# Optimization experiments

Measured on AMD Instinct MI355X. Metric: run time of the kernel, lower is better.

## Reference

```python
import jax, jax.numpy as jnp
import numpy as np
from jax import lax

CONF_THRES = 0.5
IOU_THRES = 0.45
TOP_K = 2048  # fixed candidate cap for jit-friendly NMS


def _xywh2xyxy(x):
    # x: [N,4] center-x, center-y, w, h -> x1,y1,x2,y2
    xy, wh = x[:, :2], x[:, 2:4]
    return jnp.concatenate([xy - wh / 2, xy + wh / 2], axis=-1)


def _box_iou(b1, b2):
    # b1: [N,4], b2: [M,4] in xyxy -> [N,M]
    area1 = (b1[:, 2] - b1[:, 0]) * (b1[:, 3] - b1[:, 1])
    area2 = (b2[:, 2] - b2[:, 0]) * (b2[:, 3] - b2[:, 1])
    lt = jnp.maximum(b1[:, None, :2], b2[None, :, :2])
    rb = jnp.minimum(b1[:, None, 2:], b2[None, :, 2:])
    inter = jnp.clip(rb - lt, 0).prod(-1)
    return inter / (area1[:, None] + area2[None, :] - inter)


def _nms_per_image(x):
    # x: [N,16] = xywh(4), obj(1), landmarks(10), cls_score(1); nc=1 path
    obj = x[:, 4]
    conf = x[:, 15] * obj          # x[:,15:] *= x[:,4:5], then max over 1 class
    box = _xywh2xyxy(x[:, :4])
    valid = (obj > CONF_THRES) & (conf > CONF_THRES)
    score = jnp.where(valid, conf, -jnp.inf)

    topv, topi = lax.top_k(score, TOP_K)          # sorted descending
    valid_k = jnp.isfinite(topv)                  # [K]
    boxes_k = box[topi]                           # [K,4]; class offset c = 0 (nc=1)
    x_k = x[topi]                                 # [K,16]
    conf_k = conf[topi]

    iou = _box_iou(boxes_k, boxes_k)              # [K,K]

    def body(keep, inp):
        i, iou_row, v = inp
        suppressed = jnp.any(keep & (iou_row > IOU_THRES))
        keep_i = v & ~suppressed
        return keep.at[i].set(keep_i), keep_i

    keep, _ = lax.scan(body, jnp.zeros(TOP_K, bool),
                       (jnp.arange(TOP_K), iou, valid_k))

    # detection row: [x1,y1,x2,y2, conf, 10 landmarks, class(=0)]
    det = jnp.concatenate(
        [boxes_k, conf_k[:, None], x_k[:, 5:15],
         jnp.zeros((TOP_K, 1), x.dtype)], axis=1)
    return jnp.where(keep[:, None], det, jnp.zeros((), x.dtype))


def setup_inputs() -> dict:
    key = jax.random.key(0)
    prediction = jax.random.uniform(key, (8, 100800, 16), dtype=jnp.float32)
    return {"prediction": prediction}


def reference(prediction):
    # prediction: [B, N, 16] -> padded detections [B, TOP_K, 16]
    return jax.vmap(_nms_per_image)(prediction)
```

## Files before the change

### kernel.cpp

```cpp
#include <hip/hip_runtime.h>
#include <stdint.h>

#define NA    100800
#define NIMG  8
#define TOPK  2048
#define NBLK1 99
typedef unsigned long long u64;

__global__ __launch_bounds__(256) void k1_scan(const float* __restrict__ pred,
                                               u64* __restrict__ cand,
                                               int* __restrict__ hist,
                                               int* __restrict__ cnt) {
    __shared__ int lhist[64];
    __shared__ u64 lkeys[1024];
    __shared__ int lcnt;
    __shared__ int gbase;
    int t = threadIdx.x;
    int m = blockIdx.y;
    if (t < 64) lhist[t] = 0;
    if (t == 0) lcnt = 0;
    __syncthreads();
    const float4* p4 = reinterpret_cast<const float4*>(pred + (size_t)m * NA * 16);
    int row0blk = blockIdx.x * 1024;
    for (int pass = 0; pass < 4; ++pass) {
        int row0 = row0blk + pass * 256;
        int i1 = row0 * 4 + 2 * t + 1;
        int i2 = i1 + 512;
        float4 A = make_float4(0.f, 0.f, 0.f, 0.f);
        float4 B = make_float4(0.f, 0.f, 0.f, 0.f);
        if ((i1 >> 2) < NA) A = p4[i1];
        if ((i2 >> 2) < NA) B = p4[i2];
        float aw = __shfl_xor(A.w, 1);
        float bw = __shfl_xor(B.w, 1);
        if (!(t & 1)) {
            int rA = row0 + (t >> 1);
            int rB = rA + 128;
            {
                float obj = A.x, x15 = aw;
                if (rA < NA) {
                    float conf = __fmul_rn(x15, obj);
                    if (obj > 0.5f && conf > 0.5f) {
                        unsigned cb = __float_as_uint(conf);
                        atomicAdd(&lhist[min(63, (int)((cb - 0x3F000000u) >> 17))], 1);
                        int p = atomicAdd(&lcnt, 1);
                        lkeys[p] = ((u64)cb << 32) | (u64)(0xFFFFFFFFu - (unsigned)rA);
                    }
                }
            }
            {
                float obj = B.x, x15 = bw;
                if (rB < NA) {
                    float conf = __fmul_rn(x15, obj);
                    if (obj > 0.5f && conf > 0.5f) {
                        unsigned cb = __float_as_uint(conf);
                        atomicAdd(&lhist[min(63, (int)((cb - 0x3F000000u) >> 17))], 1);
                        int p = atomicAdd(&lcnt, 1);
                        lkeys[p] = ((u64)cb << 32) | (u64)(0xFFFFFFFFu - (unsigned)rB);
                    }
                }
            }
        }
    }
    __syncthreads();
    if (t < 64 && lhist[t]) atomicAdd(&hist[(m << 6) + t], lhist[t]);
    if (t == 0) gbase = lcnt ? atomicAdd(&cnt[m], lcnt) : 0;
    __syncthreads();
    int n = lcnt;
    u64* cm = cand + (size_t)m * NA;
    for (int i = t; i < n; i += 256) cm[gbase + i] = lkeys[i];
}

__global__ __launch_bounds__(1024) void k2_rank(const u64* __restrict__ cand,
                                                const int* __restrict__ hist,
                                                const int* __restrict__ cnt,
                                                const float* __restrict__ pred,
                                                u64* __restrict__ sel,
                                                float4* __restrict__ boxes) {
    __shared__ int fcnt[4096];
    __shared__ int fstart[4096];
    __shared__ u64 outb[4096];
    __shared__ int wsum[16];
    __shared__ int cutsh, msh;
    int m = blockIdx.x, t = threadIdx.x;
    int lane = t & 63, w = t >> 6;
    if (t == 0) msh = 0;
    #pragma unroll
    for (int r = 0; r < 4; ++r) { fcnt[t + r * 1024] = 0; outb[t + r * 1024] = 0ull; }
    __syncthreads();
    if (w == 0) {
        int h = hist[(m << 6) + lane];
        #pragma unroll
        for (int off = 1; off < 64; off <<= 1) {
            int src = lane + off;
            int v = __shfl(h, src < 64 ? src : lane);
            h += (src < 64) ? v : 0;
        }
        int total  = __shfl(h, 0);
        int needed = min(total, TOPK);
        u64 bal = __ballot(h >= needed);
        int cutoff = 63 - __clzll(bal);
        if (lane == 0) cutsh = cutoff;
    }
    __syncthreads();
    int cut = cutsh;
    int count = cnt[m];
    const u64* cm = cand + (size_t)m * NA;
    for (int i = t; i < count; i += 1024) {
        u64 key = cm[i];
        unsigned cb = (unsigned)(key >> 32);
        bool keep = min(63, (int)((cb - 0x3F000000u) >> 17)) >= cut;
        u64 bal = __ballot(keep);
        if (bal) {
            int n = __popcll(bal);
            int base = 0;
            if (lane == 0) base = atomicAdd(&msh, n);
            base = __shfl(base, 0);
            if (keep) {
                int p = base + (int)__popcll(bal & ((1ull << lane) - 1ull));
                if (p < 4096) outb[p] = key;
            }
        }
    }
    __syncthreads();
    int M = min(msh, 4096);
    u64 kk[4]; int rb[4];
    #pragma unroll
    for (int r = 0; r < 4; ++r) {
        int i = t + r * 1024;
        kk[r] = 0ull; rb[r] = -1;
        if (i < M) {
            kk[r] = outb[i];
            rb[r] = 4095 - (int)(((unsigned)(kk[r] >> 32) - 0x3F000000u) >> 11);
            atomicAdd(&fcnt[rb[r]], 1);
        }
    }
    __syncthreads();
    int c0 = fcnt[4 * t], c1 = fcnt[4 * t + 1], c2 = fcnt[4 * t + 2], c3 = fcnt[4 * t + 3];
    int s = c0 + c1 + c2 + c3;
    int incl = s;
    #pragma unroll
    for (int off = 1; off < 64; off <<= 1) {
        int v = __shfl_up(incl, off);
        if (lane >= off) incl += v;
    }
    if (lane == 63) wsum[w] = incl;
    __syncthreads();
    if (w == 0) {
        int v = (lane < 16) ? wsum[lane] : 0;
        #pragma unroll
        for (int off = 1; off < 16; off <<= 1) {
            int u = __shfl_up(v, off);
            if (lane >= off) v += u;
        }
        if (lane < 16) wsum[lane] = v;
    }
    __syncthreads();
    int base = (w > 0 ? wsum[w - 1] : 0) + (incl - s);
    fstart[4 * t]     = base;
    fstart[4 * t + 1] = base + c0;
    fstart[4 * t + 2] = base + c0 + c1;
    fstart[4 * t + 3] = base + c0 + c1 + c2;
    __syncthreads();
    #pragma unroll
    for (int r = 0; r < 4; ++r) {
        if (rb[r] >= 0) {
            int old = atomicSub(&fcnt[rb[r]], 1);
            int slot = fstart[rb[r]] + old - 1;
            outb[slot] = kk[r];
        }
    }
    __syncthreads();
    #pragma unroll
    for (int r = 0; r < 4; ++r) {
        int b = t + r * 1024;
        int st = fstart[b];
        int en = (b < 4095) ? fstart[b + 1] : M;
        for (int x = st + 1; x < en; ++x) {
            u64 key = outb[x];
            int y = x - 1;
            while (y >= st && outb[y] < key) { outb[y + 1] = outb[y]; --y; }
            outb[y + 1] = key;
        }
    }
    __syncthreads();
    #pragma unroll
    for (int r = 0; r < 2; ++r) {
        int i = t + r * 1024;
        u64 key = outb[i];
        sel[(size_t)m * TOPK + i] = key;
        float4 b = make_float4(0.f, 0.f, 0.f, 0.f);
        if (key) {
            unsigned idx = 0xFFFFFFFFu - (unsigned)(key & 0xFFFFFFFFull);
            const float4* rv = reinterpret_cast<const float4*>(pred + ((size_t)m * NA + idx) * 16);
            float4 v = rv[0];
            float hw = __fmul_rn(v.z, 0.5f), hh = __fmul_rn(v.w, 0.5f);
            b.x = __fsub_rn(v.x, hw);
            b.y = __fsub_rn(v.y, hh);
            b.z = __fadd_rn(v.x, hw);
            b.w = __fadd_rn(v.y, hh);
        }
        boxes[(size_t)m * TOPK + i] = b;
    }
}

__global__ __launch_bounds__(1024) void k4_masks(const float4* __restrict__ boxes,
                                                 u64* __restrict__ maskT) {
    __shared__ float4 bx[TOPK];
    int m   = blockIdx.y;
    int grp = blockIdx.x;
    for (int i = threadIdx.x; i < TOPK; i += 1024)
        bx[i] = boxes[(size_t)m * TOPK + i];
    __syncthreads();

    int il = threadIdx.x & 31;
    int w  = threadIdx.x >> 5;
    int i  = grp * 32 + il;
    float4 b1 = bx[i];
    float a1 = __fmul_rn(__fsub_rn(b1.z, b1.x), __fsub_rn(b1.w, b1.y));
    u64 bits = 0ull;
    #pragma unroll 4
    for (int jj = 0; jj < 64; ++jj) {
        float4 b2 = bx[w * 64 + jj];
        float a2 = __fmul_rn(__fsub_rn(b2.z, b2.x), __fsub_rn(b2.w, b2.y));
        float iw = fmaxf(__fsub_rn(fminf(b1.z, b2.z), fmaxf(b1.x, b2.x)), 0.f);
        float ih = fmaxf(__fsub_rn(fminf(b1.w, b2.w), fmaxf(b1.y, b2.y)), 0.f);
        float inter = __fmul_rn(iw, ih);
        float uni   = __fsub_rn(__fadd_rn(a1, a2), inter);
        float iou   = __fdiv_rn(inter, uni);
        if (iou > 0.45f) bits |= (1ull << jj);
    }
    maskT[((size_t)m * 32 + w) * 2048 + i] = bits;
}

__global__ __launch_bounds__(1024) void k5_nms(const u64* __restrict__ sel,
                                               const u64* __restrict__ maskT,
                                               const float* __restrict__ pred,
                                               float4* __restrict__ out) {
    __shared__ u64 remv[32];
    __shared__ u64 kbshare[2];
    __shared__ u64 kws[32];
    int m = blockIdx.x;
    int t = threadIdx.x;
    int lane = t & 63;
    int wv = t >> 6;
    const u64* mt = maskT + (size_t)m * 32 * 2048;
    if (t < 32) remv[t] = 0ull;
    u64 dval = 0ull, sval = 0ull, tval = 0ull;
    u64 cfmask = 0ull;
    u64 mybit = 1ull << lane;
    u64 lowmask = mybit - 1ull;
    if (wv == 0) {
        dval = mt[(size_t)0 * 2048 + lane];
        sval = sel[(size_t)m * TOPK + lane];
        tval = mt[(size_t)0 * 2048 + 64 + lane];
    }
    __syncthreads();

    u64 uA1 = 0ull, uA2 = 0ull, uB1 = 0ull, uB2 = 0ull;

#define K5_SCAN(B) do {                                                       \
    u64 dn = 0ull, sn = 0ull, tn = 0ull;                                      \
    if ((B) < 31) {                                                           \
        int r = ((B) + 1) * 64 + lane;                                        \
        dn = mt[(size_t)((B) + 1) * 2048 + r];                                \
        sn = sel[(size_t)m * TOPK + r];                                       \
        if ((B) < 30) tn = mt[(size_t)((B) + 1) * 2048 + r + 64];             \
    }                                                                         \
    u64 ext = remv[(B)];                                                      \
    u64 validw = __ballot(sval != 0ull);                                      \
    u64 alive = validw & ~ext & ~cfmask;                                      \
    u64 kb = 0ull;                                                            \
    while (alive) {                                                           \
        u64 c = dval & alive & lowmask;                                       \
        u64 ready = __ballot(((alive & mybit) != 0ull) && (c == 0ull));       \
        kb |= ready;                                                          \
        u64 removed = __ballot((dval & ready) != 0ull);                       \
        alive &= ~(ready | removed);                                          \
    }                                                                         \
    cfmask = ((B) < 31) ? __ballot((tval & kb) != 0ull) : 0ull;               \
    if (lane == 0) { kbshare[(B) & 1] = kb; kws[(B)] = kb; }                  \
    dval = dn; sval = sn; tval = tn;                                          \
} while (0)

#define K5_UP_ISSUE(V1, V2, S) do {           \
    int w1_ = (S) + wv, w2_ = (S) + 15 + wv;                                  \
    V1 = (w1_ < 32) ? mt[(size_t)((S) - 1) * 2048 + w1_ * 64 + lane] : 0ull;  \
    V2 = (w2_ < 32) ? mt[(size_t)((S) - 1) * 2048 + w2_ * 64 + lane] : 0ull;  \
} while (0)

#define K5_UP_CONSUME(V1, V2, B) do {                                         \
    u64 kb = kbshare[((B) - 1) & 1];                                          \
    int w1_ = (B) + wv, w2_ = (B) + 15 + wv;                                  \
    u64 c1 = __ballot((V1 & kb) != 0ull);                                     \
    u64 c2 = __ballot((V2 & kb) != 0ull);                                     \
    if (w1_ < 32 && lane == 0) remv[w1_] |= c1;                               \
    if (w2_ < 32 && lane == 0) remv[w2_] |= c2;                               \
} while (0)

    #pragma unroll 1
    for (int it = 0; it < 16; ++it) {
        int b0 = 2 * it, b1 = b0 + 1;
        if (wv == 0) {
            K5_SCAN(b0);
        } else {
            K5_UP_ISSUE(uB1, uB2, b0 + 1);
            if (b0 >= 1) K5_UP_CONSUME(uA1, uA2, b0);
        }
        __syncthreads();
        if (wv == 0) {
            K5_SCAN(b1);
        } else {
            if (b1 + 1 < 32) K5_UP_ISSUE(uA1, uA2, b1 + 1);
            K5_UP_CONSUME(uB1, uB2, b1);
        }
        __syncthreads();
    }
#undef K5_SCAN
#undef K5_UP_ISSUE
#undef K5_UP_CONSUME

    const u64* sl = sel + (size_t)m * TOPK;
    float4* om = out + (size_t)m * TOPK * 4;
    #pragma unroll
    for (int q = t; q < TOPK * 4; q += 1024) {
        int c4 = q & 3;
        int r  = q >> 2;
        float4 o = make_float4(0.f, 0.f, 0.f, 0.f);
        if ((kws[r >> 6] >> (r & 63)) & 1ull) {
            u64 key = sl[r];
            unsigned idx = 0xFFFFFFFFu - (unsigned)(key & 0xFFFFFFFFull);
            const float4* rv = reinterpret_cast<const float4*>(pred + ((size_t)m * NA + idx) * 16);
            float4 v = rv[c4];
            if (c4 == 0) {
                float hw = __fmul_rn(v.z, 0.5f), hh = __fmul_rn(v.w, 0.5f);
                o = make_float4(__fsub_rn(v.x, hw), __fsub_rn(v.y, hh),
                                __fadd_rn(v.x, hw), __fadd_rn(v.y, hh));
            } else if (c4 == 1) {
                o = make_float4(__uint_as_float((unsigned)(key >> 32)), v.y, v.z, v.w);
            } else if (c4 == 2) {
                o = v;
            } else {
                o = make_float4(v.x, v.y, v.z, 0.f);
            }
        }
        om[q] = o;
    }
}

extern "C" void kernel_launch(void* const* d_in, const int* in_sizes, int n_in,
                              void* d_out, int out_size, void* d_ws, size_t ws_size,
                              hipStream_t stream) {
    (void)in_sizes; (void)n_in; (void)out_size; (void)ws_size;
    const float* pred = (const float*)d_in[0];
    char* ws = (char*)d_ws;
    u64*      cand     = (u64*)     (ws + 0);
    u64*      sel      = (u64*)     (ws + 6451200);
    float4*   boxes    = (float4*)  (ws + 6582272);
    u64*      maskT    = (u64*)     (ws + 6844416);
    int*      hist     = (int*)     (ws + 11038720);
    int*      cnt      = (int*)     (ws + 11040768);
    float4*   out      = (float4*)d_out;

    hipMemsetAsync(hist, 0, 2048 + 32, stream);
    hipLaunchKernelGGL(k1_scan,  dim3(NBLK1, NIMG), dim3(256),  0, stream, pred, cand, hist, cnt);
    hipLaunchKernelGGL(k2_rank,  dim3(NIMG),        dim3(1024), 0, stream, cand, hist, cnt, pred, sel, boxes);
    hipLaunchKernelGGL(k4_masks, dim3(64, NIMG),    dim3(1024), 0, stream, boxes, maskT);
    hipLaunchKernelGGL(k5_nms,   dim3(NIMG),        dim3(1024), 0, stream, sel, maskT, pred, out);
}
```

Measured before the change: 94.61 us.

## Replace global atomics with per-block histograms and shrink NMS block to 512

k1 now writes each block's 64-bin histogram and candidate count to per-block slots, and stores its keys at a fixed per-block offset instead of reserving space with global atomics. This removes the memset launch and atomic contention. k2 reduces the per-block histograms itself and walks the 99 segments, paying one extra pass with a per-segment loop that leaves most threads idle. Separately, k5 drops to 512 threads, and each updater wave now handles up to 5 mask words at stride 7 instead of 2, cutting the cost of each block-wide barrier.

```diff
diff --git a/kernel.cpp b/kernel.cpp
--- a/kernel.cpp
+++ b/kernel.cpp
@@ -9,19 +9,19 @@
 
 __global__ __launch_bounds__(256) void k1_scan(const float* __restrict__ pred,
                                                u64* __restrict__ cand,
-                                               int* __restrict__ hist,
-                                               int* __restrict__ cnt) {
+                                               int* __restrict__ histb,
+                                               int* __restrict__ bcnt) {
     __shared__ int lhist[64];
     __shared__ u64 lkeys[1024];
     __shared__ int lcnt;
-    __shared__ int gbase;
     int t = threadIdx.x;
     int m = blockIdx.y;
+    int b = blockIdx.x;
     if (t < 64) lhist[t] = 0;
     if (t == 0) lcnt = 0;
     __syncthreads();
     const float4* p4 = reinterpret_cast<const float4*>(pred + (size_t)m * NA * 16);
-    int row0blk = blockIdx.x * 1024;
+    int row0blk = b * 1024;
     for (int pass = 0; pass < 4; ++pass) {
         int row0 = row0blk + pass * 256;
         int i1 = row0 * 4 + 2 * t + 1;
@@ -62,20 +62,20 @@
         }
     }
     __syncthreads();
-    if (t < 64 && lhist[t]) atomicAdd(&hist[(m << 6) + t], lhist[t]);
-    if (t == 0) gbase = lcnt ? atomicAdd(&cnt[m], lcnt) : 0;
-    __syncthreads();
+    if (t < 64) histb[((size_t)m * NBLK1 + b) * 64 + t] = lhist[t];
+    if (t == 0) bcnt[m * NBLK1 + b] = lcnt;
     int n = lcnt;
-    u64* cm = cand + (size_t)m * NA;
-    for (int i = t; i < n; i += 256) cm[gbase + i] = lkeys[i];
+    u64* cm = cand + (size_t)m * NA + (size_t)b * 1024;
+    for (int i = t; i < n; i += 256) cm[i] = lkeys[i];
 }
 
 __global__ __launch_bounds__(1024) void k2_rank(const u64* __restrict__ cand,
-                                                const int* __restrict__ hist,
-                                                const int* __restrict__ cnt,
+                                                const int* __restrict__ histb,
+                                                const int* __restrict__ bcnt,
                                                 const float* __restrict__ pred,
                                                 u64* __restrict__ sel,
                                                 float4* __restrict__ boxes) {
+    __shared__ int lhist[64];
     __shared__ int fcnt[4096];
     __shared__ int fstart[4096];
     __shared__ u64 outb[4096];
@@ -83,12 +83,20 @@
     __shared__ int cutsh, msh;
     int m = blockIdx.x, t = threadIdx.x;
     int lane = t & 63, w = t >> 6;
+    if (t < 64) lhist[t] = 0;
     if (t == 0) msh = 0;
     #pragma unroll
     for (int r = 0; r < 4; ++r) { fcnt[t + r * 1024] = 0; outb[t + r * 1024] = 0ull; }
     __syncthreads();
+    {
+        int s = 0;
+        for (int b = w; b < NBLK1; b += 16)
+            s += histb[((size_t)m * NBLK1 + b) * 64 + lane];
+        if (s) atomicAdd(&lhist[lane], s);
+    }
+    __syncthreads();
     if (w == 0) {
-        int h = hist[(m << 6) + lane];
+        int h = lhist[lane];
         #pragma unroll
         for (int off = 1; off < 64; off <<= 1) {
             int src = lane + off;
@@ -103,17 +111,21 @@
     }
     __syncthreads();
     int cut = cutsh;
-    int count = cnt[m];
     const u64* cm = cand + (size_t)m * NA;
-    for (int i = t; i < count; i += 1024) {
-        u64 key = cm[i];
-        unsigned cb = (unsigned)(key >> 32);
-        bool keep = min(63, (int)((cb - 0x3F000000u) >> 17)) >= cut;
+    for (int seg = 0; seg < NBLK1; ++seg) {
+        int n = bcnt[m * NBLK1 + seg];
+        u64 key = 0ull;
+        bool keep = false;
+        if (t < n) {
+            key = cm[(size_t)seg * 1024 + t];
+            unsigned cb = (unsigned)(key >> 32);
+            keep = min(63, (int)((cb - 0x3F000000u) >> 17)) >= cut;
+        }
         u64 bal = __ballot(keep);
         if (bal) {
-            int n = __popcll(bal);
+            int c = __popcll(bal);
             int base = 0;
-            if (lane == 0) base = atomicAdd(&msh, n);
+            if (lane == 0) base = atomicAdd(&msh, c);
             base = __shfl(base, 0);
             if (keep) {
                 int p = base + (int)__popcll(bal & ((1ull << lane) - 1ull));
@@ -232,10 +244,10 @@
     maskT[((size_t)m * 32 + w) * 2048 + i] = bits;
 }
 
-__global__ __launch_bounds__(1024) void k5_nms(const u64* __restrict__ sel,
-                                               const u64* __restrict__ maskT,
-                                               const float* __restrict__ pred,
-                                               float4* __restrict__ out) {
+__global__ __launch_bounds__(512) void k5_nms(const u64* __restrict__ sel,
+                                              const u64* __restrict__ maskT,
+                                              const float* __restrict__ pred,
+                                              float4* __restrict__ out) {
     __shared__ u64 remv[32];
     __shared__ u64 kbshare[2];
     __shared__ u64 kws[32];
@@ -256,7 +268,9 @@
     }
     __syncthreads();
 
-    u64 uA1 = 0ull, uA2 = 0ull, uB1 = 0ull, uB2 = 0ull;
+    u64 uA[5], uB[5];
+    #pragma unroll
+    for (int k = 0; k < 5; ++k) { uA[k] = 0ull; uB[k] = 0ull; }
 
 #define K5_SCAN(B) do {                                                       \
     u64 dn = 0ull, sn = 0ull, tn = 0ull;                                      \
@@ -282,19 +296,22 @@
     dval = dn; sval = sn; tval = tn;                                          \
 } while (0)
 
-#define K5_UP_ISSUE(V1, V2, S) do {           \
-    int w1_ = (S) + wv, w2_ = (S) + 15 + wv;                                  \
-    V1 = (w1_ < 32) ? mt[(size_t)((S) - 1) * 2048 + w1_ * 64 + lane] : 0ull;  \
-    V2 = (w2_ < 32) ? mt[(size_t)((S) - 1) * 2048 + w2_ * 64 + lane] : 0ull;  \
+#define K5_UP_ISSUE(V, S) do {   \
+    _Pragma("unroll")                                                         \
+    for (int k = 0; k < 5; ++k) {                                             \
+        int w_ = (S) + wv + 7 * k;                                            \
+        V[k] = (w_ < 32) ? mt[(size_t)((S) - 1) * 2048 + w_ * 64 + lane] : 0ull; \
+    }                                                                         \
 } while (0)
 
-#define K5_UP_CONSUME(V1, V2, B) do {                                         \
+#define K5_UP_CONSUME(V, B) do {                                              \
     u64 kb = kbshare[((B) - 1) & 1];                                          \
-    int w1_ = (B) + wv, w2_ = (B) + 15 + wv;                                  \
-    u64 c1 = __ballot((V1 & kb) != 0ull);                                     \
-    u64 c2 = __ballot((V2 & kb) != 0ull);                                     \
-    if (w1_ < 32 && lane == 0) remv[w1_] |= c1;                               \
-    if (w2_ < 32 && lane == 0) remv[w2_] |= c2;                               \
+    _Pragma("unroll")                                                         \
+    for (int k = 0; k < 5; ++k) {                                             \
+        int w_ = (B) + wv + 7 * k;                                            \
+        u64 c_ = __ballot((V[k] & kb) != 0ull);                               \
+        if (w_ < 32 && lane == 0) remv[w_] |= c_;                             \
+    }                                                                         \
 } while (0)
 
     #pragma unroll 1
@@ -303,15 +320,15 @@
         if (wv == 0) {
             K5_SCAN(b0);
         } else {
-            K5_UP_ISSUE(uB1, uB2, b0 + 1);
-            if (b0 >= 1) K5_UP_CONSUME(uA1, uA2, b0);
+            K5_UP_ISSUE(uB, b0 + 1);
+            if (b0 >= 1) K5_UP_CONSUME(uA, b0);
         }
         __syncthreads();
         if (wv == 0) {
             K5_SCAN(b1);
         } else {
-            if (b1 + 1 < 32) K5_UP_ISSUE(uA1, uA2, b1 + 1);
-            K5_UP_CONSUME(uB1, uB2, b1);
+            if (b1 + 1 < 32) K5_UP_ISSUE(uA, b1 + 1);
+            K5_UP_CONSUME(uB, b1);
         }
         __syncthreads();
     }
@@ -322,7 +339,7 @@
     const u64* sl = sel + (size_t)m * TOPK;
     float4* om = out + (size_t)m * TOPK * 4;
     #pragma unroll
-    for (int q = t; q < TOPK * 4; q += 1024) {
+    for (int q = t; q < TOPK * 4; q += 512) {
         int c4 = q & 3;
         int r  = q >> 2;
         float4 o = make_float4(0.f, 0.f, 0.f, 0.f);
@@ -357,13 +374,12 @@
     u64*      sel      = (u64*)     (ws + 6451200);
     float4*   boxes    = (float4*)  (ws + 6582272);
     u64*      maskT    = (u64*)     (ws + 6844416);
-    int*      hist     = (int*)     (ws + 11038720);
-    int*      cnt      = (int*)     (ws + 11040768);
+    int*      histb    = (int*)     (ws + 11038720);
+    int*      bcnt     = (int*)     (ws + 11241472);
     float4*   out      = (float4*)d_out;
 
-    hipMemsetAsync(hist, 0, 2048 + 32, stream);
-    hipLaunchKernelGGL(k1_scan,  dim3(NBLK1, NIMG), dim3(256),  0, stream, pred, cand, hist, cnt);
-    hipLaunchKernelGGL(k2_rank,  dim3(NIMG),        dim3(1024), 0, stream, cand, hist, cnt, pred, sel, boxes);
+    hipLaunchKernelGGL(k1_scan,  dim3(NBLK1, NIMG), dim3(256),  0, stream, pred, cand, histb, bcnt);
+    hipLaunchKernelGGL(k2_rank,  dim3(NIMG),        dim3(1024), 0, stream, cand, histb, bcnt, pred, sel, boxes);
     hipLaunchKernelGGL(k4_masks, dim3(64, NIMG),    dim3(1024), 0, stream, boxes, maskT);
-    hipLaunchKernelGGL(k5_nms,   dim3(NIMG),        dim3(1024), 0, stream, sel, maskT, pred, out);
-}
+    hipLaunchKernelGGL(k5_nms,   dim3(NIMG),        dim3(512),  0, stream, sel, maskT, pred, out);
+}
```

After: 126.4 us. +33.6%, slower.

## Replace global histogram and atomics with per-block segment counts and two-pass bucket ranking

Applied to the files above, without the earlier changes.

The scan kernel stops building a coarse global histogram and appending candidates through a global atomic. Each block now writes its candidates to a fixed segment and records its own count, which removes the memset and the global atomics. The rank kernel prefix-sums the block counts and reads every candidate twice through a binary search over segments. It counts fine buckets, finds the bucket holding the top-K cutoff, then scatters and sorts only buckets at or above that cutoff. The cost is a second full read of the candidates in a single block per image, where the old version read them once.

```diff
diff --git a/kernel.cpp b/kernel.cpp
--- a/kernel.cpp
+++ b/kernel.cpp
@@ -5,23 +5,21 @@
 #define NIMG  8
 #define TOPK  2048
 #define NBLK1 99
+#define SEGSTRIDE (NBLK1 * 1024)
 typedef unsigned long long u64;
 
 __global__ __launch_bounds__(256) void k1_scan(const float* __restrict__ pred,
                                                u64* __restrict__ cand,
-                                               int* __restrict__ hist,
-                                               int* __restrict__ cnt) {
-    __shared__ int lhist[64];
+                                               int* __restrict__ bcnt) {
     __shared__ u64 lkeys[1024];
     __shared__ int lcnt;
-    __shared__ int gbase;
     int t = threadIdx.x;
     int m = blockIdx.y;
-    if (t < 64) lhist[t] = 0;
+    int b = blockIdx.x;
     if (t == 0) lcnt = 0;
     __syncthreads();
     const float4* p4 = reinterpret_cast<const float4*>(pred + (size_t)m * NA * 16);
-    int row0blk = blockIdx.x * 1024;
+    int row0blk = b * 1024;
     for (int pass = 0; pass < 4; ++pass) {
         int row0 = row0blk + pass * 256;
         int i1 = row0 * 4 + 2 * t + 1;
@@ -41,7 +39,6 @@
                     float conf = __fmul_rn(x15, obj);
                     if (obj > 0.5f && conf > 0.5f) {
                         unsigned cb = __float_as_uint(conf);
-                        atomicAdd(&lhist[min(63, (int)((cb - 0x3F000000u) >> 17))], 1);
                         int p = atomicAdd(&lcnt, 1);
                         lkeys[p] = ((u64)cb << 32) | (u64)(0xFFFFFFFFu - (unsigned)rA);
                     }
@@ -53,7 +50,6 @@
                     float conf = __fmul_rn(x15, obj);
                     if (obj > 0.5f && conf > 0.5f) {
                         unsigned cb = __float_as_uint(conf);
-                        atomicAdd(&lhist[min(63, (int)((cb - 0x3F000000u) >> 17))], 1);
                         int p = atomicAdd(&lcnt, 1);
                         lkeys[p] = ((u64)cb << 32) | (u64)(0xFFFFFFFFu - (unsigned)rB);
                     }
@@ -62,17 +58,14 @@
         }
     }
     __syncthreads();
-    if (t < 64 && lhist[t]) atomicAdd(&hist[(m << 6) + t], lhist[t]);
-    if (t == 0) gbase = lcnt ? atomicAdd(&cnt[m], lcnt) : 0;
-    __syncthreads();
+    if (t == 0) bcnt[m * NBLK1 + b] = lcnt;
     int n = lcnt;
-    u64* cm = cand + (size_t)m * NA;
-    for (int i = t; i < n; i += 256) cm[gbase + i] = lkeys[i];
+    u64* cm = cand + (size_t)m * SEGSTRIDE + (size_t)b * 1024;
+    for (int i = t; i < n; i += 256) cm[i] = lkeys[i];
 }
 
 __global__ __launch_bounds__(1024) void k2_rank(const u64* __restrict__ cand,
-                                                const int* __restrict__ hist,
-                                                const int* __restrict__ cnt,
+                                                const int* __restrict__ bcnt,
                                                 const float* __restrict__ pred,
                                                 u64* __restrict__ sel,
                                                 float4* __restrict__ boxes) {
@@ -80,59 +73,46 @@
     __shared__ int fstart[4096];
     __shared__ u64 outb[4096];
     __shared__ int wsum[16];
-    __shared__ int cutsh, msh;
+    __shared__ int P[100];
+    __shared__ int bstar_sh, toplim_sh;
     int m = blockIdx.x, t = threadIdx.x;
     int lane = t & 63, w = t >> 6;
-    if (t == 0) msh = 0;
+    if (t == 0) { bstar_sh = -1; toplim_sh = 0; }
     #pragma unroll
     for (int r = 0; r < 4; ++r) { fcnt[t + r * 1024] = 0; outb[t + r * 1024] = 0ull; }
     __syncthreads();
     if (w == 0) {
-        int h = hist[(m << 6) + lane];
+        const int* bb = bcnt + m * NBLK1;
+        int s1 = bb[lane];
         #pragma unroll
         for (int off = 1; off < 64; off <<= 1) {
-            int src = lane + off;
-            int v = __shfl(h, src < 64 ? src : lane);
-            h += (src < 64) ? v : 0;
-        }
-        int total  = __shfl(h, 0);
-        int needed = min(total, TOPK);
-        u64 bal = __ballot(h >= needed);
-        int cutoff = 63 - __clzll(bal);
-        if (lane == 0) cutsh = cutoff;
-    }
-    __syncthreads();
-    int cut = cutsh;
-    int count = cnt[m];
-    const u64* cm = cand + (size_t)m * NA;
-    for (int i = t; i < count; i += 1024) {
-        u64 key = cm[i];
-        unsigned cb = (unsigned)(key >> 32);
-        bool keep = min(63, (int)((cb - 0x3F000000u) >> 17)) >= cut;
-        u64 bal = __ballot(keep);
-        if (bal) {
-            int n = __popcll(bal);
-            int base = 0;
-            if (lane == 0) base = atomicAdd(&msh, n);
-            base = __shfl(base, 0);
-            if (keep) {
-                int p = base + (int)__popcll(bal & ((1ull << lane) - 1ull));
-                if (p < 4096) outb[p] = key;
-            }
-        }
-    }
-    __syncthreads();
-    int M = min(msh, 4096);
-    u64 kk[4]; int rb[4];
-    #pragma unroll
-    for (int r = 0; r < 4; ++r) {
-        int i = t + r * 1024;
-        kk[r] = 0ull; rb[r] = -1;
-        if (i < M) {
-            kk[r] = outb[i];
-            rb[r] = 4095 - (int)(((unsigned)(kk[r] >> 32) - 0x3F000000u) >> 11);
-            atomicAdd(&fcnt[rb[r]], 1);
-        }
+            int u = __shfl_up(s1, off);
+            if (lane >= off) s1 += u;
+        }
+        P[lane + 1] = s1;
+        if (lane == 0) P[0] = 0;
+        int tot1 = __shfl(s1, 63);
+        int s2 = (lane < 35) ? bb[64 + lane] : 0;
+        #pragma unroll
+        for (int off = 1; off < 64; off <<= 1) {
+            int u = __shfl_up(s2, off);
+            if (lane >= off) s2 += u;
+        }
+        if (lane < 35) P[65 + lane] = s2 + tot1;
+    }
+    __syncthreads();
+    int M = P[99];
+    int need = min(M, TOPK);
+    for (int d = t; d < M; d += 1024) {
+        int lo = 0, hi = 99;
+        #pragma unroll
+        for (int it = 0; it < 7; ++it) {
+            int mid = (lo + hi) >> 1;
+            if (P[mid] <= d) lo = mid; else hi = mid;
+        }
+        u64 key = cand[(size_t)m * SEGSTRIDE + (size_t)lo * 1024 + (d - P[lo])];
+        int rb = 4095 - (int)(((unsigned)(key >> 32) - 0x3F000000u) >> 11);
+        atomicAdd(&fcnt[rb], 1);
     }
     __syncthreads();
     int c0 = fcnt[4 * t], c1 = fcnt[4 * t + 1], c2 = fcnt[4 * t + 2], c3 = fcnt[4 * t + 3];
@@ -156,30 +136,48 @@
     }
     __syncthreads();
     int base = (w > 0 ? wsum[w - 1] : 0) + (incl - s);
+    int e0 = base + c0, e1 = e0 + c1, e2 = e1 + c2, e3 = e2 + c3;
     fstart[4 * t]     = base;
-    fstart[4 * t + 1] = base + c0;
-    fstart[4 * t + 2] = base + c0 + c1;
-    fstart[4 * t + 3] = base + c0 + c1 + c2;
-    __syncthreads();
-    #pragma unroll
-    for (int r = 0; r < 4; ++r) {
-        if (rb[r] >= 0) {
-            int old = atomicSub(&fcnt[rb[r]], 1);
-            int slot = fstart[rb[r]] + old - 1;
-            outb[slot] = kk[r];
+    fstart[4 * t + 1] = e0;
+    fstart[4 * t + 2] = e1;
+    fstart[4 * t + 3] = e2;
+    if (need > 0) {
+        if (base < need && e0 >= need) { bstar_sh = 4 * t;     toplim_sh = min(e0, 4096); }
+        if (e0   < need && e1 >= need) { bstar_sh = 4 * t + 1; toplim_sh = min(e1, 4096); }
+        if (e1   < need && e2 >= need) { bstar_sh = 4 * t + 2; toplim_sh = min(e2, 4096); }
+        if (e2   < need && e3 >= need) { bstar_sh = 4 * t + 3; toplim_sh = min(e3, 4096); }
+    }
+    __syncthreads();
+    int bstar = bstar_sh, toplim = toplim_sh;
+    for (int d = t; d < M; d += 1024) {
+        int lo = 0, hi = 99;
+        #pragma unroll
+        for (int it = 0; it < 7; ++it) {
+            int mid = (lo + hi) >> 1;
+            if (P[mid] <= d) lo = mid; else hi = mid;
+        }
+        u64 key = cand[(size_t)m * SEGSTRIDE + (size_t)lo * 1024 + (d - P[lo])];
+        int rb = 4095 - (int)(((unsigned)(key >> 32) - 0x3F000000u) >> 11);
+        if (rb <= bstar) {
+            int old = atomicSub(&fcnt[rb], 1);
+            int slot = fstart[rb] + old - 1;
+            if (slot < 4096) outb[slot] = key;
         }
     }
     __syncthreads();
     #pragma unroll
     for (int r = 0; r < 4; ++r) {
         int b = t + r * 1024;
-        int st = fstart[b];
-        int en = (b < 4095) ? fstart[b + 1] : M;
-        for (int x = st + 1; x < en; ++x) {
-            u64 key = outb[x];
-            int y = x - 1;
-            while (y >= st && outb[y] < key) { outb[y + 1] = outb[y]; --y; }
-            outb[y + 1] = key;
+        if (b <= bstar) {
+            int st = fstart[b];
+            int en = (b < bstar) ? fstart[b + 1] : toplim;
+            if (en > 4096) en = 4096;
+            for (int x = st + 1; x < en; ++x) {
+                u64 key = outb[x];
+                int y = x - 1;
+                while (y >= st && outb[y] < key) { outb[y + 1] = outb[y]; --y; }
+                outb[y + 1] = key;
+            }
         }
     }
     __syncthreads();
@@ -354,16 +352,14 @@
     const float* pred = (const float*)d_in[0];
     char* ws = (char*)d_ws;
     u64*      cand     = (u64*)     (ws + 0);
-    u64*      sel      = (u64*)     (ws + 6451200);
-    float4*   boxes    = (float4*)  (ws + 6582272);
-    u64*      maskT    = (u64*)     (ws + 6844416);
-    int*      hist     = (int*)     (ws + 11038720);
-    int*      cnt      = (int*)     (ws + 11040768);
+    u64*      sel      = (u64*)     (ws + 6488064);
+    float4*   boxes    = (float4*)  (ws + 6619136);
+    u64*      maskT    = (u64*)     (ws + 6881280);
+    int*      bcnt     = (int*)     (ws + 11075584);
     float4*   out      = (float4*)d_out;
 
-    hipMemsetAsync(hist, 0, 2048 + 32, stream);
-    hipLaunchKernelGGL(k1_scan,  dim3(NBLK1, NIMG), dim3(256),  0, stream, pred, cand, hist, cnt);
-    hipLaunchKernelGGL(k2_rank,  dim3(NIMG),        dim3(1024), 0, stream, cand, hist, cnt, pred, sel, boxes);
+    hipLaunchKernelGGL(k1_scan,  dim3(NBLK1, NIMG), dim3(256),  0, stream, pred, cand, bcnt);
+    hipLaunchKernelGGL(k2_rank,  dim3(NIMG),        dim3(1024), 0, stream, cand, bcnt, pred, sel, boxes);
     hipLaunchKernelGGL(k4_masks, dim3(64, NIMG),    dim3(1024), 0, stream, boxes, maskT);
     hipLaunchKernelGGL(k5_nms,   dim3(NIMG),        dim3(1024), 0, stream, sel, maskT, pred, out);
 }
```

After: 93.37 us, median of 2. Within noise of the previous version (-1.3%).
